# Performance work log

Measured on AMD Instinct MI355X. Metric: run time of the kernel, lower is better.

Reference implementation:

```python
import jax, jax.numpy as jnp
import numpy as np

B, D, L = 8, 512, 8192


def log_g(x):
    # th.where(x >= 0, log(relu(x) + 1), x)
    return jnp.where(x >= 0, jnp.log1p(jnp.maximum(x, 0.0)), x)


def min_gru(hg):
    # hg: [B, H, L] -> [B, H/2, L]
    h, gate = jnp.split(hg, 2, axis=1)
    log_coeffs = -jax.nn.softplus(gate)                      # log a_t
    log_values = -jax.nn.softplus(-gate) + log_g(h)          # log b_t
    a_star = jnp.cumsum(log_coeffs, axis=2)
    log_h0_plus_b_star = jax.lax.cumlogsumexp(log_values - a_star, axis=2)
    return jnp.exp(a_star + log_h0_plus_b_star)


def conv1x1(x, w, b):
    # x: [B, D, L], w: [E, D], b: [E]  (kernel-size-1 Conv1d == pointwise linear)
    return jnp.einsum('ed,bdl->bel', w, x) + b[None, :, None]


def setup_inputs() -> dict:
    key = jax.random.key(0)
    k1, k2, k3, k4, k5 = jax.random.split(key, 5)
    scale = 1.0 / np.sqrt(D)
    x = jax.random.normal(k1, (B, D, L), dtype=jnp.float32)
    w_fore = jax.random.normal(k2, (D, D), dtype=jnp.float32) * scale
    b_fore = jax.random.normal(k3, (D,), dtype=jnp.float32) * scale
    w_back = jax.random.normal(k4, (D, D), dtype=jnp.float32) * scale
    b_back = jax.random.normal(k5, (D,), dtype=jnp.float32) * scale
    return {'x': x, 'w_fore': w_fore, 'b_fore': b_fore, 'w_back': w_back, 'b_back': b_back}


def reference(x, w_fore, b_fore, w_back, b_back):
    fore = min_gru(conv1x1(x, w_fore, b_fore))                            # [B, D/2, L]
    back = jnp.flip(min_gru(conv1x1(jnp.flip(x, 2), w_back, b_back)), 2)  # [B, D/2, L]
    return jnp.concatenate([fore, back], axis=1)                          # [B, D, L]
```

## Files before the change

kernel.cpp:

```cpp
#include <hip/hip_runtime.h>

#define BATCH 8
#define DIN   512
#define SEQ   8192
#define ECH   1024
#define HCH   256
#define CL    32
#define NCHNK (SEQ / CL)
#define NSC   16

typedef __bf16 bf16;
typedef __bf16 bf16x8 __attribute__((ext_vector_type(8)));
typedef __bf16 bf16x4 __attribute__((ext_vector_type(4)));
typedef float  floatx4 __attribute__((ext_vector_type(4)));

__device__ __forceinline__ void async_ld16(void* lds, const void* g) {
  __builtin_amdgcn_global_load_lds(
      (const __attribute__((address_space(1))) unsigned int*)g,
      (__attribute__((address_space(3))) unsigned int*)lds, 16, 0, 0);
}

__device__ __forceinline__ float bits2f(unsigned u) {
  return __builtin_bit_cast(float, u);
}

__device__ __forceinline__ void gru_ab(unsigned v, float& a, float& bt) {
  float hh = bits2f(v << 16);
  float g  = bits2f(v & 0xffff0000u);
  float eg = __expf(-g);
  float sg = 1.f / (1.f + eg);
  a = eg * sg;
  float gv = hh >= 0.f ? 1.f + hh : __expf(hh);
  bt = sg * gv;
}

__global__ void k_wconv(const float* __restrict__ wf, const float* __restrict__ bfo,
                        const float* __restrict__ wb, const float* __restrict__ bb,
                        bf16* __restrict__ Wb, float* __restrict__ bias) {
  int idx = blockIdx.x * 256 + threadIdx.x;
  if (idx < ECH * DIN) {
    int n = idx >> 9, d = idx & 511;
    int dir = n >> 9, r = n & 511, e = r >> 1, isg = r & 1;
    int s = e + (isg ? HCH : 0);
    const float* w = dir ? wb : wf;
    Wb[idx] = (bf16)w[s * DIN + d];
  }
  if (idx < ECH) {
    int dir = idx >> 9, r = idx & 511, e = r >> 1, isg = r & 1;
    int s = e + (isg ? HCH : 0);
    bias[idx] = (dir ? bb : bfo)[s];
  }
}

__global__ void k_xpose(const float* __restrict__ x, bf16* __restrict__ xT) {
  __shared__ float T[64 * 65];
  int t = threadIdx.x;
  int l0 = blockIdx.x * 64;
  int d0 = blockIdx.y * 64;
  int b  = blockIdx.z;
  const float* xb = x + (size_t)b * DIN * SEQ;
#pragma unroll
  for (int p = 0; p < 4; ++p) {
    int dl = (t >> 4) + p * 16;
    int l4 = (t & 15) * 4;
    float4 v = *(const float4*)(xb + (size_t)(d0 + dl) * SEQ + l0 + l4);
    T[dl * 65 + l4 + 0] = v.x;
    T[dl * 65 + l4 + 1] = v.y;
    T[dl * 65 + l4 + 2] = v.z;
    T[dl * 65 + l4 + 3] = v.w;
  }
  __syncthreads();
  bf16* xTb = xT + (size_t)b * SEQ * DIN;
#pragma unroll
  for (int p = 0; p < 2; ++p) {
    int ll = (t >> 3) + p * 32;
    int d8 = (t & 7) * 8;
    bf16x8 h;
#pragma unroll
    for (int j = 0; j < 8; ++j) h[j] = (bf16)T[(d8 + j) * 65 + ll];
    *(bf16x8*)(xTb + (size_t)(l0 + ll) * DIN + d0 + d8) = h;
  }
}

__launch_bounds__(256, 4)
__global__ void k_gemm(const bf16* __restrict__ xT, const bf16* __restrict__ Wb,
                       const float* __restrict__ bias, bf16* __restrict__ hg,
                       float* __restrict__ Asum, float* __restrict__ Bsum) {
  __shared__ bf16 lds[16896];
  bf16* As = lds;
  bf16* Bs = lds + 8192;

  int t = threadIdx.x;
  int lane = t & 63, wave = t >> 6;

  int lin = blockIdx.x + 8 * blockIdx.y;
  int xcd = lin & 7;
  int seq = lin >> 3;
  int ltile = xcd + 8 * (seq >> 3);
  int ntile = seq & 7;
  int n0 = ntile * 128;
  int l0 = ltile * 128;
  int b  = blockIdx.z;

  int l15 = lane & 15, quad = lane >> 4;
  int wm = wave >> 1, wn = wave & 1;
  int mb = wm * 64, nb = wn * 64;

  const bf16* gA = xT + ((size_t)b * SEQ + l0) * DIN;
  const bf16* gB = Wb + (size_t)n0 * DIN;

  int srow = wave * 32 + (lane >> 3);
  int scol = (((lane & 7) ^ (lane >> 3)) * 8);

  floatx4 acc[4][4];
#pragma unroll
  for (int i = 0; i < 4; ++i)
#pragma unroll
    for (int j = 0; j < 4; ++j) acc[i][j] = (floatx4){0.f, 0.f, 0.f, 0.f};

  for (int kt = 0; kt < DIN / 64; ++kt) {
    int k0 = kt * 64;
#pragma unroll
    for (int q = 0; q < 4; ++q) {
      async_ld16(As + (wave * 32 + q * 8) * 64,
                 gA + (size_t)(srow + q * 8) * DIN + k0 + scol);
      async_ld16(Bs + (wave * 32 + q * 8) * 64,
                 gB + (size_t)(srow + q * 8) * DIN + k0 + scol);
    }
    __syncthreads();
#pragma unroll
    for (int kk = 0; kk < 64; kk += 32) {
      int rsw = l15 & 7;
      bf16x8 af[4], bfr[4];
#pragma unroll
      for (int i = 0; i < 4; ++i)
        af[i] = *(const bf16x8*)(As + (mb + i * 16 + l15) * 64 +
                                 (((kk >> 3) + quad) ^ rsw) * 8);
#pragma unroll
      for (int i = 0; i < 4; ++i)
        bfr[i] = *(const bf16x8*)(Bs + (nb + i * 16 + l15) * 64 +
                                  (((kk >> 3) + quad) ^ rsw) * 8);
#pragma unroll
      for (int mi = 0; mi < 4; ++mi)
#pragma unroll
        for (int ni = 0; ni < 4; ++ni)
          acc[mi][ni] = __builtin_amdgcn_mfma_f32_16x16x32_bf16(
              af[mi], bfr[ni], acc[mi][ni], 0, 0, 0);
    }
    __syncthreads();
  }

  float bb4[4];
#pragma unroll
  for (int ni = 0; ni < 4; ++ni) bb4[ni] = bias[n0 + nb + ni * 16 + l15];
  bf16* Cs = lds;
#pragma unroll
  for (int mi = 0; mi < 4; ++mi)
#pragma unroll
    for (int ni = 0; ni < 4; ++ni)
#pragma unroll
      for (int r = 0; r < 4; ++r) {
        int row = mb + mi * 16 + quad * 4 + r;
        int col = nb + ni * 16 + l15;
        Cs[row * 132 + col] = (bf16)(acc[mi][ni][r] + bb4[ni]);
      }
  __syncthreads();
  bf16* hgb = hg + ((size_t)b * SEQ + l0) * ECH + n0;
#pragma unroll
  for (int p = 0; p < 8; ++p) {
    int row = p * 16 + (t >> 4);
    int seg = t & 15;
    *(bf16x8*)(hgb + (size_t)row * ECH + seg * 8) =
        *(const bf16x8*)(Cs + row * 132 + seg * 8);
  }

  {
    int dirn = ntile >> 2;
    int c = wave, el = lane;
    float A = 1.f, Bc = 0.f;
#pragma unroll 8
    for (int i = 0; i < CL; ++i) {
      int row = c * CL + (dirn ? (CL - 1 - i) : i);
      unsigned v = *(const unsigned*)(Cs + row * 132 + 2 * el);
      float a, bt;
      gru_ab(v, a, bt);
      A *= a;
      Bc = a * Bc + bt;
    }
    int chunkg = ltile * 4 + c;
    int eg = ((n0 & 511) >> 1) + el;
    size_t o = ((size_t)(b * 2 + dirn) * NCHNK + chunkg) * 256 + eg;
    Asum[o] = A;
    Bsum[o] = Bc;
  }
}

__global__ void k_scan2a(const float* __restrict__ Asum, const float* __restrict__ Bsum,
                         float* __restrict__ SA, float* __restrict__ SB) {
  int e = threadIdx.x, sc = blockIdx.x, row2 = blockIdx.y, dir = row2 & 1;
  size_t base = (size_t)row2 * NCHNK;
  float Acc = 1.f, Bcc = 0.f;
#pragma unroll
  for (int i = 0; i < 16; ++i) {
    int c = sc * 16 + (dir ? 15 - i : i);
    size_t o = (base + c) * 256 + e;
    float a = Asum[o], bv = Bsum[o];
    Acc = a * Acc;
    Bcc = a * Bcc + bv;
  }
  size_t so = ((size_t)row2 * NSC + sc) * 256 + e;
  SA[so] = Acc;
  SB[so] = Bcc;
}

__global__ void k_scan2b(const float* __restrict__ SA, const float* __restrict__ SB,
                         float* __restrict__ hsc) {
  int e = threadIdx.x, row2 = blockIdx.x, dir = row2 & 1;
  float h = 0.f;
  for (int i = 0; i < NSC; ++i) {
    int sc = dir ? NSC - 1 - i : i;
    size_t o = ((size_t)row2 * NSC + sc) * 256 + e;
    hsc[o] = h;
    h = SA[o] * h + SB[o];
  }
}

__global__ void k_scan2c(const float* __restrict__ Asum, const float* __restrict__ Bsum,
                         const float* __restrict__ hsc, float* __restrict__ hin) {
  int e = threadIdx.x, sc = blockIdx.x, row2 = blockIdx.y, dir = row2 & 1;
  float h = hsc[((size_t)row2 * NSC + sc) * 256 + e];
#pragma unroll
  for (int i = 0; i < 16; ++i) {
    int c = sc * 16 + (dir ? 15 - i : i);
    size_t o = ((size_t)row2 * NCHNK + c) * 256 + e;
    hin[o] = h;
    h = Asum[o] * h + Bsum[o];
  }
}

__global__ void k_scan3(const bf16* __restrict__ hg, const float* __restrict__ hin,
                        float* __restrict__ out) {
  __shared__ float T[256 * 33];
  int t = threadIdx.x;
  int chunk = blockIdx.x, dir = blockIdx.y, b = blockIdx.z;
  const bf16* hb = hg + (size_t)b * SEQ * ECH + dir * 512 + 2 * t;
  float h = hin[((size_t)(b * 2 + dir) * NCHNK + chunk) * 256 + t];
  int lbase = chunk * CL;
#pragma unroll 8
  for (int i = 0; i < CL; ++i) {
    int ll = dir ? (CL - 1 - i) : i;
    unsigned v = *(const unsigned*)(hb + (size_t)(lbase + ll) * ECH);
    float a, bt;
    gru_ab(v, a, bt);
    h = a * h + bt;
    T[t * 33 + ll] = h;
  }
  __syncthreads();
  float* ob = out + ((size_t)b * 512 + dir * 256) * SEQ + lbase;
#pragma unroll
  for (int p = 0; p < 8; ++p) {
    int row = p * 32 + (t >> 3);
    int c4 = (t & 7) * 4;
    float4 v4;
    v4.x = T[row * 33 + c4 + 0];
    v4.y = T[row * 33 + c4 + 1];
    v4.z = T[row * 33 + c4 + 2];
    v4.w = T[row * 33 + c4 + 3];
    *(float4*)(ob + (size_t)row * SEQ + c4) = v4;
  }
}

extern "C" void kernel_launch(void* const* d_in, const int* in_sizes, int n_in,
                              void* d_out, int out_size, void* d_ws, size_t ws_size,
                              hipStream_t stream) {
  const float* x   = (const float*)d_in[0];
  const float* wf  = (const float*)d_in[1];
  const float* bfo = (const float*)d_in[2];
  const float* wb  = (const float*)d_in[3];
  const float* bb  = (const float*)d_in[4];
  float* out = (float*)d_out;
  char* ws = (char*)d_ws;

  bf16*  xT   = (bf16*)(ws);
  bf16*  hg   = (bf16*)(ws + 67108864);
  bf16*  Wbm  = (bf16*)(ws + 201326592);
  float* bias = (float*)(ws + 202375168);
  float* Asum = (float*)(ws + 202379264);
  float* Bsum = (float*)(ws + 206573568);
  float* hin  = (float*)(ws + 210767872);
  float* SA   = (float*)(ws + 214962176);
  float* SB   = (float*)(ws + 215224320);
  float* hsc  = (float*)(ws + 215486464);

  k_wconv<<<2048, 256, 0, stream>>>(wf, bfo, wb, bb, Wbm, bias);
  k_xpose<<<dim3(SEQ / 64, DIN / 64, BATCH), 256, 0, stream>>>(x, xT);
  k_gemm<<<dim3(ECH / 128, SEQ / 128, BATCH), 256, 0, stream>>>(xT, Wbm, bias, hg,
                                                                Asum, Bsum);
  k_scan2a<<<dim3(NSC, 16), 256, 0, stream>>>(Asum, Bsum, SA, SB);
  k_scan2b<<<16, 256, 0, stream>>>(SA, SB, hsc);
  k_scan2c<<<dim3(NSC, 16), 256, 0, stream>>>(Asum, Bsum, hsc, hin);
  k_scan3<<<dim3(NCHNK, 2, BATCH), 256, 0, stream>>>(hg, hin, out);
}
```

Baseline: 372.0 us.

## Enlarge GEMM tile to 256x256 with 4-stage async LDS pipeline

The GEMM kernel moves from 128x128 tiles with 256 threads and a single-buffered K loop to 256x256 tiles with 512 threads. The K loop now uses BK=32 with a 4-deep ring of LDS buffers, prefetching three stages ahead with explicit vmcnt waits and raised wave priority around the MFMAs. The aim is to overlap global loads with matrix math and to increase operand reuse per tile. In exchange it uses far more LDS and registers, which lowers occupancy. The LDS layout drops the XOR swizzle, which risks bank conflicts, and the chunk-summary epilogue is remapped to the larger tile.

```diff
diff --git a/kernel.cpp b/kernel.cpp
--- a/kernel.cpp
+++ b/kernel.cpp
@@ -11,7 +11,6 @@
 
 typedef __bf16 bf16;
 typedef __bf16 bf16x8 __attribute__((ext_vector_type(8)));
-typedef __bf16 bf16x4 __attribute__((ext_vector_type(4)));
 typedef float  floatx4 __attribute__((ext_vector_type(4)));
 
 __device__ __forceinline__ void async_ld16(void* lds, const void* g) {
@@ -82,113 +81,129 @@
   }
 }
 
-__launch_bounds__(256, 4)
+#define BKK 32
+#define NKT (DIN / BKK)
+#define CS_STRIDE 268
+
+__launch_bounds__(512, 2)
 __global__ void k_gemm(const bf16* __restrict__ xT, const bf16* __restrict__ Wb,
                        const float* __restrict__ bias, bf16* __restrict__ hg,
                        float* __restrict__ Asum, float* __restrict__ Bsum) {
-  __shared__ bf16 lds[16896];
-  bf16* As = lds;
-  bf16* Bs = lds + 8192;
+  __shared__ __align__(16) bf16 lds[68608];
 
   int t = threadIdx.x;
   int lane = t & 63, wave = t >> 6;
-
-  int lin = blockIdx.x + 8 * blockIdx.y;
-  int xcd = lin & 7;
-  int seq = lin >> 3;
-  int ltile = xcd + 8 * (seq >> 3);
-  int ntile = seq & 7;
-  int n0 = ntile * 128;
-  int l0 = ltile * 128;
+  int l15 = lane & 15, quad = lane >> 4;
+  int wm = wave >> 2, wn = wave & 3;
+
+  int lin = blockIdx.x + 4 * blockIdx.y;
+  int swz = (lin & 7) * 16 + (lin >> 3);
+  int ntile = swz & 3, ltile = swz >> 2;
+  int n0 = ntile * 256;
+  int l0 = ltile * 256;
   int b  = blockIdx.z;
-
-  int l15 = lane & 15, quad = lane >> 4;
-  int wm = wave >> 1, wn = wave & 1;
-  int mb = wm * 64, nb = wn * 64;
 
   const bf16* gA = xT + ((size_t)b * SEQ + l0) * DIN;
   const bf16* gB = Wb + (size_t)n0 * DIN;
 
-  int srow = wave * 32 + (lane >> 3);
-  int scol = (((lane & 7) ^ (lane >> 3)) * 8);
-
-  floatx4 acc[4][4];
-#pragma unroll
-  for (int i = 0; i < 4; ++i)
+  int srow = t >> 2;
+  int scol = (t & 3) * 8;
+
+  float bb4[4];
+#pragma unroll
+  for (int ni = 0; ni < 4; ++ni) bb4[ni] = bias[n0 + wn * 64 + ni * 16 + l15];
+
+#define STAGE(KT) do {                                                     \
+    bf16* dst = lds + ((KT) & 3) * 16384 + t * 8;                          \
+    const bf16* sA = gA + (size_t)srow * DIN + (KT) * BKK + scol;          \
+    const bf16* sB = gB + (size_t)srow * DIN + (KT) * BKK + scol;          \
+    async_ld16(dst,         sA);                                           \
+    async_ld16(dst + 4096,  sA + (size_t)128 * DIN);                       \
+    async_ld16(dst + 8192,  sB);                                           \
+    async_ld16(dst + 12288, sB + (size_t)128 * DIN);                       \
+  } while (0)
+
+  STAGE(0); STAGE(1); STAGE(2);
+
+  floatx4 acc[8][4];
+#pragma unroll
+  for (int i = 0; i < 8; ++i)
 #pragma unroll
     for (int j = 0; j < 4; ++j) acc[i][j] = (floatx4){0.f, 0.f, 0.f, 0.f};
 
-  for (int kt = 0; kt < DIN / 64; ++kt) {
-    int k0 = kt * 64;
-#pragma unroll
-    for (int q = 0; q < 4; ++q) {
-      async_ld16(As + (wave * 32 + q * 8) * 64,
-                 gA + (size_t)(srow + q * 8) * DIN + k0 + scol);
-      async_ld16(Bs + (wave * 32 + q * 8) * 64,
-                 gB + (size_t)(srow + q * 8) * DIN + k0 + scol);
-    }
-    __syncthreads();
-#pragma unroll
-    for (int kk = 0; kk < 64; kk += 32) {
-      int rsw = l15 & 7;
-      bf16x8 af[4], bfr[4];
-#pragma unroll
-      for (int i = 0; i < 4; ++i)
-        af[i] = *(const bf16x8*)(As + (mb + i * 16 + l15) * 64 +
-                                 (((kk >> 3) + quad) ^ rsw) * 8);
-#pragma unroll
-      for (int i = 0; i < 4; ++i)
-        bfr[i] = *(const bf16x8*)(Bs + (nb + i * 16 + l15) * 64 +
-                                  (((kk >> 3) + quad) ^ rsw) * 8);
-#pragma unroll
-      for (int mi = 0; mi < 4; ++mi)
-#pragma unroll
-        for (int ni = 0; ni < 4; ++ni)
-          acc[mi][ni] = __builtin_amdgcn_mfma_f32_16x16x32_bf16(
-              af[mi], bfr[ni], acc[mi][ni], 0, 0, 0);
-    }
-    __syncthreads();
-  }
-
-  float bb4[4];
-#pragma unroll
-  for (int ni = 0; ni < 4; ++ni) bb4[ni] = bias[n0 + nb + ni * 16 + l15];
+#pragma unroll
+  for (int kt = 0; kt < NKT; ++kt) {
+    if (kt <= NKT - 3)      asm volatile("s_waitcnt vmcnt(8)" ::: "memory");
+    else if (kt == NKT - 2) asm volatile("s_waitcnt vmcnt(4)" ::: "memory");
+    else                    asm volatile("s_waitcnt vmcnt(0)" ::: "memory");
+    __builtin_amdgcn_s_barrier();
+    asm volatile("" ::: "memory");
+
+    if (kt + 3 < NKT) STAGE(kt + 3);
+
+    const bf16* As = lds + (kt & 3) * 16384;
+    const bf16* Bs = As + 8192;
+    bf16x8 af[8], bfr[4];
+#pragma unroll
+    for (int i = 0; i < 8; ++i)
+      af[i] = *(const bf16x8*)(As + (wm * 128 + i * 16 + l15) * BKK + quad * 8);
+#pragma unroll
+    for (int i = 0; i < 4; ++i)
+      bfr[i] = *(const bf16x8*)(Bs + (wn * 64 + i * 16 + l15) * BKK + quad * 8);
+
+    __builtin_amdgcn_s_setprio(1);
+#pragma unroll
+    for (int mi = 0; mi < 8; ++mi)
+#pragma unroll
+      for (int ni = 0; ni < 4; ++ni)
+        acc[mi][ni] = __builtin_amdgcn_mfma_f32_16x16x32_bf16(
+            af[mi], bfr[ni], acc[mi][ni], 0, 0, 0);
+    __builtin_amdgcn_s_setprio(0);
+  }
+#undef STAGE
+
+  __syncthreads();
+
   bf16* Cs = lds;
 #pragma unroll
-  for (int mi = 0; mi < 4; ++mi)
+  for (int mi = 0; mi < 8; ++mi)
 #pragma unroll
     for (int ni = 0; ni < 4; ++ni)
 #pragma unroll
       for (int r = 0; r < 4; ++r) {
-        int row = mb + mi * 16 + quad * 4 + r;
-        int col = nb + ni * 16 + l15;
-        Cs[row * 132 + col] = (bf16)(acc[mi][ni][r] + bb4[ni]);
+        int row = wm * 128 + mi * 16 + quad * 4 + r;
+        int col = wn * 64 + ni * 16 + l15;
+        Cs[row * CS_STRIDE + col] = (bf16)(acc[mi][ni][r] + bb4[ni]);
       }
   __syncthreads();
+
   bf16* hgb = hg + ((size_t)b * SEQ + l0) * ECH + n0;
 #pragma unroll
-  for (int p = 0; p < 8; ++p) {
-    int row = p * 16 + (t >> 4);
-    int seg = t & 15;
+  for (int p = 0; p < 16; ++p) {
+    int row = p * 16 + (t >> 5);
+    int seg = t & 31;
     *(bf16x8*)(hgb + (size_t)row * ECH + seg * 8) =
-        *(const bf16x8*)(Cs + row * 132 + seg * 8);
-  }
-
-  {
-    int dirn = ntile >> 2;
-    int c = wave, el = lane;
+        *(const bf16x8*)(Cs + row * CS_STRIDE + seg * 8);
+  }
+
+  int dirn = ntile >> 1;
+#pragma unroll
+  for (int j = 0; j < 2; ++j) {
+    int u = t + j * 512;
+    int c = u >> 7;
+    int e = u & 127;
     float A = 1.f, Bc = 0.f;
 #pragma unroll 8
     for (int i = 0; i < CL; ++i) {
       int row = c * CL + (dirn ? (CL - 1 - i) : i);
-      unsigned v = *(const unsigned*)(Cs + row * 132 + 2 * el);
+      unsigned v = *(const unsigned*)(Cs + row * CS_STRIDE + 2 * e);
       float a, bt;
       gru_ab(v, a, bt);
       A *= a;
       Bc = a * Bc + bt;
     }
-    int chunkg = ltile * 4 + c;
-    int eg = ((n0 & 511) >> 1) + el;
+    int chunkg = ltile * 8 + c;
+    int eg = (ntile & 1) * 128 + e;
     size_t o = ((size_t)(b * 2 + dirn) * NCHNK + chunkg) * 256 + eg;
     Asum[o] = A;
     Bsum[o] = Bc;
@@ -294,7 +309,7 @@
 
   k_wconv<<<2048, 256, 0, stream>>>(wf, bfo, wb, bb, Wbm, bias);
   k_xpose<<<dim3(SEQ / 64, DIN / 64, BATCH), 256, 0, stream>>>(x, xT);
-  k_gemm<<<dim3(ECH / 128, SEQ / 128, BATCH), 256, 0, stream>>>(xT, Wbm, bias, hg,
+  k_gemm<<<dim3(ECH / 256, SEQ / 256, BATCH), 512, 0, stream>>>(xT, Wbm, bias, hg,
                                                                 Asum, Bsum);
   k_scan2a<<<dim3(NSC, 16), 256, 0, stream>>>(Asum, Bsum, SA, SB);
   k_scan2b<<<16, 256, 0, stream>>>(SA, SB, hsc);
```

Result: slower. 390.2 us (+4.9%).

## Load pre-fragmented weights directly to registers and merge scan kernels into one

Applied to the files above, without the earlier changes.

The weight conversion kernel now writes W in an MFMA-fragment-ordered layout, so the GEMM loads B operands from global straight into registers instead of staging them through LDS. The LDS traffic and async loads for W are removed. The K loop is fully unrolled and the bias load is hoisted ahead of it. The three-kernel hierarchical chunk scan is replaced by one sequential kernel over all 256 chunks, with only 16 blocks. That saves two launches but makes a long serial loop with little parallelism.

```diff
diff --git a/kernel.cpp b/kernel.cpp
--- a/kernel.cpp
+++ b/kernel.cpp
@@ -11,7 +11,6 @@
 
 typedef __bf16 bf16;
 typedef __bf16 bf16x8 __attribute__((ext_vector_type(8)));
-typedef __bf16 bf16x4 __attribute__((ext_vector_type(4)));
 typedef float  floatx4 __attribute__((ext_vector_type(4)));
 
 __device__ __forceinline__ void async_ld16(void* lds, const void* g) {
@@ -36,14 +35,16 @@
 
 __global__ void k_wconv(const float* __restrict__ wf, const float* __restrict__ bfo,
                         const float* __restrict__ wb, const float* __restrict__ bb,
-                        bf16* __restrict__ Wb, float* __restrict__ bias) {
+                        bf16* __restrict__ Wf, float* __restrict__ bias) {
   int idx = blockIdx.x * 256 + threadIdx.x;
   if (idx < ECH * DIN) {
     int n = idx >> 9, d = idx & 511;
     int dir = n >> 9, r = n & 511, e = r >> 1, isg = r & 1;
     int s = e + (isg ? HCH : 0);
     const float* w = dir ? wb : wf;
-    Wb[idx] = (bf16)w[s * DIN + d];
+    size_t o = ((size_t)((n >> 4) * 16 + (d >> 5)) << 9) +
+               ((((d >> 3) & 3) * 16 + (n & 15)) << 3) + (d & 7);
+    Wf[o] = (bf16)w[s * DIN + d];
   }
   if (idx < ECH) {
     int dir = idx >> 9, r = idx & 511, e = r >> 1, isg = r & 1;
@@ -82,16 +83,21 @@
   }
 }
 
+#define BKK 64
+#define NKT (DIN / BKK)
+
 __launch_bounds__(256, 4)
-__global__ void k_gemm(const bf16* __restrict__ xT, const bf16* __restrict__ Wb,
+__global__ void k_gemm(const bf16* __restrict__ xT, const bf16* __restrict__ Wf,
                        const float* __restrict__ bias, bf16* __restrict__ hg,
                        float* __restrict__ Asum, float* __restrict__ Bsum) {
-  __shared__ bf16 lds[16896];
+  __shared__ __align__(16) bf16 lds[16896];
   bf16* As = lds;
-  bf16* Bs = lds + 8192;
 
   int t = threadIdx.x;
   int lane = t & 63, wave = t >> 6;
+  int l15 = lane & 15, quad = lane >> 4, rsw = l15 & 7;
+  int wm = wave >> 1, wn = wave & 1;
+  int mb = wm * 64, nb = wn * 64;
 
   int lin = blockIdx.x + 8 * blockIdx.y;
   int xcd = lin & 7;
@@ -102,15 +108,15 @@
   int l0 = ltile * 128;
   int b  = blockIdx.z;
 
-  int l15 = lane & 15, quad = lane >> 4;
-  int wm = wave >> 1, wn = wave & 1;
-  int mb = wm * 64, nb = wn * 64;
-
   const bf16* gA = xT + ((size_t)b * SEQ + l0) * DIN;
-  const bf16* gB = Wb + (size_t)n0 * DIN;
+  int nb16 = (n0 >> 4) + wn * 4;
+
+  float bb4[4];
+#pragma unroll
+  for (int ni = 0; ni < 4; ++ni) bb4[ni] = bias[n0 + nb + ni * 16 + l15];
 
   int srow = wave * 32 + (lane >> 3);
-  int scol = (((lane & 7) ^ (lane >> 3)) * 8);
+  int scol = ((lane & 7) ^ ((lane >> 3) & 7)) * 8;
 
   floatx4 acc[4][4];
 #pragma unroll
@@ -118,41 +124,41 @@
 #pragma unroll
     for (int j = 0; j < 4; ++j) acc[i][j] = (floatx4){0.f, 0.f, 0.f, 0.f};
 
-  for (int kt = 0; kt < DIN / 64; ++kt) {
-    int k0 = kt * 64;
-#pragma unroll
-    for (int q = 0; q < 4; ++q) {
+#pragma unroll
+  for (int kt = 0; kt < NKT; ++kt) {
+    int k0 = kt * BKK;
+#pragma unroll
+    for (int q = 0; q < 4; ++q)
       async_ld16(As + (wave * 32 + q * 8) * 64,
                  gA + (size_t)(srow + q * 8) * DIN + k0 + scol);
-      async_ld16(Bs + (wave * 32 + q * 8) * 64,
-                 gB + (size_t)(srow + q * 8) * DIN + k0 + scol);
+
+    bf16x8 bfr[4][2];
+#pragma unroll
+    for (int i = 0; i < 4; ++i)
+#pragma unroll
+      for (int k2 = 0; k2 < 2; ++k2)
+        bfr[i][k2] = *(const bf16x8*)(Wf +
+            (((size_t)(nb16 + i) * 16 + kt * 2 + k2) << 9) + lane * 8);
+
+    __syncthreads();
+
+#pragma unroll
+    for (int k2 = 0; k2 < 2; ++k2) {
+      bf16x8 af[4];
+#pragma unroll
+      for (int i = 0; i < 4; ++i)
+        af[i] = *(const bf16x8*)(As + (mb + i * 16 + l15) * 64 +
+                                 (((k2 * 4 + quad) ^ rsw) * 8));
+#pragma unroll
+      for (int mi = 0; mi < 4; ++mi)
+#pragma unroll
+        for (int ni = 0; ni < 4; ++ni)
+          acc[mi][ni] = __builtin_amdgcn_mfma_f32_16x16x32_bf16(
+              af[mi], bfr[ni][k2], acc[mi][ni], 0, 0, 0);
     }
     __syncthreads();
-#pragma unroll
-    for (int kk = 0; kk < 64; kk += 32) {
-      int rsw = l15 & 7;
-      bf16x8 af[4], bfr[4];
-#pragma unroll
-      for (int i = 0; i < 4; ++i)
-        af[i] = *(const bf16x8*)(As + (mb + i * 16 + l15) * 64 +
-                                 (((kk >> 3) + quad) ^ rsw) * 8);
-#pragma unroll
-      for (int i = 0; i < 4; ++i)
-        bfr[i] = *(const bf16x8*)(Bs + (nb + i * 16 + l15) * 64 +
-                                  (((kk >> 3) + quad) ^ rsw) * 8);
-#pragma unroll
-      for (int mi = 0; mi < 4; ++mi)
-#pragma unroll
-        for (int ni = 0; ni < 4; ++ni)
-          acc[mi][ni] = __builtin_amdgcn_mfma_f32_16x16x32_bf16(
-              af[mi], bfr[ni], acc[mi][ni], 0, 0, 0);
-    }
-    __syncthreads();
-  }
-
-  float bb4[4];
-#pragma unroll
-  for (int ni = 0; ni < 4; ++ni) bb4[ni] = bias[n0 + nb + ni * 16 + l15];
+  }
+
   bf16* Cs = lds;
 #pragma unroll
   for (int mi = 0; mi < 4; ++mi)
@@ -195,44 +201,15 @@
   }
 }
 
-__global__ void k_scan2a(const float* __restrict__ Asum, const float* __restrict__ Bsum,
-                         float* __restrict__ SA, float* __restrict__ SB) {
-  int e = threadIdx.x, sc = blockIdx.x, row2 = blockIdx.y, dir = row2 & 1;
+__global__ void k_scan2(const float* __restrict__ Asum, const float* __restrict__ Bsum,
+                        float* __restrict__ hin) {
+  int e = threadIdx.x, row2 = blockIdx.x, dir = row2 & 1;
   size_t base = (size_t)row2 * NCHNK;
-  float Acc = 1.f, Bcc = 0.f;
-#pragma unroll
-  for (int i = 0; i < 16; ++i) {
-    int c = sc * 16 + (dir ? 15 - i : i);
+  float h = 0.f;
+#pragma unroll 8
+  for (int i = 0; i < NCHNK; ++i) {
+    int c = dir ? (NCHNK - 1 - i) : i;
     size_t o = (base + c) * 256 + e;
-    float a = Asum[o], bv = Bsum[o];
-    Acc = a * Acc;
-    Bcc = a * Bcc + bv;
-  }
-  size_t so = ((size_t)row2 * NSC + sc) * 256 + e;
-  SA[so] = Acc;
-  SB[so] = Bcc;
-}
-
-__global__ void k_scan2b(const float* __restrict__ SA, const float* __restrict__ SB,
-                         float* __restrict__ hsc) {
-  int e = threadIdx.x, row2 = blockIdx.x, dir = row2 & 1;
-  float h = 0.f;
-  for (int i = 0; i < NSC; ++i) {
-    int sc = dir ? NSC - 1 - i : i;
-    size_t o = ((size_t)row2 * NSC + sc) * 256 + e;
-    hsc[o] = h;
-    h = SA[o] * h + SB[o];
-  }
-}
-
-__global__ void k_scan2c(const float* __restrict__ Asum, const float* __restrict__ Bsum,
-                         const float* __restrict__ hsc, float* __restrict__ hin) {
-  int e = threadIdx.x, sc = blockIdx.x, row2 = blockIdx.y, dir = row2 & 1;
-  float h = hsc[((size_t)row2 * NSC + sc) * 256 + e];
-#pragma unroll
-  for (int i = 0; i < 16; ++i) {
-    int c = sc * 16 + (dir ? 15 - i : i);
-    size_t o = ((size_t)row2 * NCHNK + c) * 256 + e;
     hin[o] = h;
     h = Asum[o] * h + Bsum[o];
   }
@@ -283,21 +260,16 @@
 
   bf16*  xT   = (bf16*)(ws);
   bf16*  hg   = (bf16*)(ws + 67108864);
-  bf16*  Wbm  = (bf16*)(ws + 201326592);
+  bf16*  Wfm  = (bf16*)(ws + 201326592);
   float* bias = (float*)(ws + 202375168);
   float* Asum = (float*)(ws + 202379264);
   float* Bsum = (float*)(ws + 206573568);
   float* hin  = (float*)(ws + 210767872);
-  float* SA   = (float*)(ws + 214962176);
-  float* SB   = (float*)(ws + 215224320);
-  float* hsc  = (float*)(ws + 215486464);
-
-  k_wconv<<<2048, 256, 0, stream>>>(wf, bfo, wb, bb, Wbm, bias);
+
+  k_wconv<<<2048, 256, 0, stream>>>(wf, bfo, wb, bb, Wfm, bias);
   k_xpose<<<dim3(SEQ / 64, DIN / 64, BATCH), 256, 0, stream>>>(x, xT);
-  k_gemm<<<dim3(ECH / 128, SEQ / 128, BATCH), 256, 0, stream>>>(xT, Wbm, bias, hg,
+  k_gemm<<<dim3(ECH / 128, SEQ / 128, BATCH), 256, 0, stream>>>(xT, Wfm, bias, hg,
                                                                 Asum, Bsum);
-  k_scan2a<<<dim3(NSC, 16), 256, 0, stream>>>(Asum, Bsum, SA, SB);
-  k_scan2b<<<16, 256, 0, stream>>>(SA, SB, hsc);
-  k_scan2c<<<dim3(NSC, 16), 256, 0, stream>>>(Asum, Bsum, hsc, hin);
+  k_scan2<<<16, 256, 0, stream>>>(Asum, Bsum, hin);
   k_scan3<<<dim3(NCHNK, 2, BATCH), 256, 0, stream>>>(hg, hin, out);
 }
```

New measurement: 497.4 us. 33.7% more time.

## Pre-swizzle weights into MFMA fragment layout and read B operand directly from global

Applied to the files above, without the earlier changes.

The weight conversion now writes W in a per-16-row fragment order, so each GEMM wave can load its B operands straight from global/L2 into registers instead of staging them through LDS. The K tile grows to 128, with only the activation tile staged in a 16-way XOR-swizzled LDS layout, and B loads for the second half are issued between MFMA batches. The weight conversion and the x transpose are merged into one launch to save a kernel launch. The cost is more register pressure (launch bounds drop to 3 waves per SIMD) and global-latency exposure on the B loads.

```diff
diff --git a/kernel.cpp b/kernel.cpp
--- a/kernel.cpp
+++ b/kernel.cpp
@@ -11,7 +11,6 @@
 
 typedef __bf16 bf16;
 typedef __bf16 bf16x8 __attribute__((ext_vector_type(8)));
-typedef __bf16 bf16x4 __attribute__((ext_vector_type(4)));
 typedef float  floatx4 __attribute__((ext_vector_type(4)));
 
 __device__ __forceinline__ void async_ld16(void* lds, const void* g) {
@@ -34,30 +33,36 @@
   bt = sg * gv;
 }
 
-__global__ void k_wconv(const float* __restrict__ wf, const float* __restrict__ bfo,
-                        const float* __restrict__ wb, const float* __restrict__ bb,
-                        bf16* __restrict__ Wb, float* __restrict__ bias) {
-  int idx = blockIdx.x * 256 + threadIdx.x;
-  if (idx < ECH * DIN) {
-    int n = idx >> 9, d = idx & 511;
-    int dir = n >> 9, r = n & 511, e = r >> 1, isg = r & 1;
-    int s = e + (isg ? HCH : 0);
-    const float* w = dir ? wb : wf;
-    Wb[idx] = (bf16)w[s * DIN + d];
-  }
-  if (idx < ECH) {
-    int dir = idx >> 9, r = idx & 511, e = r >> 1, isg = r & 1;
-    int s = e + (isg ? HCH : 0);
-    bias[idx] = (dir ? bb : bfo)[s];
-  }
-}
-
-__global__ void k_xpose(const float* __restrict__ x, bf16* __restrict__ xT) {
+__global__ void k_prep(const float* __restrict__ x,
+                       const float* __restrict__ wf, const float* __restrict__ bfo,
+                       const float* __restrict__ wb, const float* __restrict__ bb,
+                       bf16* __restrict__ xT, bf16* __restrict__ Wf,
+                       float* __restrict__ bias) {
   __shared__ float T[64 * 65];
+  int bid = blockIdx.x;
   int t = threadIdx.x;
-  int l0 = blockIdx.x * 64;
-  int d0 = blockIdx.y * 64;
-  int b  = blockIdx.z;
+  if (bid < 2048) {
+    int idx = bid * 256 + t;
+    if (idx < ECH * DIN) {
+      int n = idx >> 9, d = idx & 511;
+      int dir = n >> 9, r = n & 511, e = r >> 1, isg = r & 1;
+      int s = e + (isg ? HCH : 0);
+      const float* w = dir ? wb : wf;
+      size_t o = ((size_t)((n >> 4) * 16 + (d >> 5)) << 9) +
+                 ((((d >> 3) & 3) * 16 + (n & 15)) << 3) + (d & 7);
+      Wf[o] = (bf16)w[s * DIN + d];
+    }
+    if (idx < ECH) {
+      int dir = idx >> 9, r = idx & 511, e = r >> 1, isg = r & 1;
+      int s = e + (isg ? HCH : 0);
+      bias[idx] = (dir ? bb : bfo)[s];
+    }
+    return;
+  }
+  int id = bid - 2048;
+  int l0 = (id & 127) * 64;
+  int d0 = ((id >> 7) & 7) * 64;
+  int b  = id >> 10;
   const float* xb = x + (size_t)b * DIN * SEQ;
 #pragma unroll
   for (int p = 0; p < 4; ++p) {
@@ -82,16 +87,21 @@
   }
 }
 
-__launch_bounds__(256, 4)
-__global__ void k_gemm(const bf16* __restrict__ xT, const bf16* __restrict__ Wb,
+#define BKK 128
+#define NKT (DIN / BKK)
+
+__launch_bounds__(256, 3)
+__global__ void k_gemm(const bf16* __restrict__ xT, const bf16* __restrict__ Wf,
                        const float* __restrict__ bias, bf16* __restrict__ hg,
                        float* __restrict__ Asum, float* __restrict__ Bsum) {
-  __shared__ bf16 lds[16896];
+  __shared__ __align__(16) bf16 lds[16896];
   bf16* As = lds;
-  bf16* Bs = lds + 8192;
 
   int t = threadIdx.x;
   int lane = t & 63, wave = t >> 6;
+  int l15 = lane & 15, quad = lane >> 4;
+  int wm = wave >> 1, wn = wave & 1;
+  int mb = wm * 64, nb = wn * 64;
 
   int lin = blockIdx.x + 8 * blockIdx.y;
   int xcd = lin & 7;
@@ -102,15 +112,12 @@
   int l0 = ltile * 128;
   int b  = blockIdx.z;
 
-  int l15 = lane & 15, quad = lane >> 4;
-  int wm = wave >> 1, wn = wave & 1;
-  int mb = wm * 64, nb = wn * 64;
-
   const bf16* gA = xT + ((size_t)b * SEQ + l0) * DIN;
-  const bf16* gB = Wb + (size_t)n0 * DIN;
-
-  int srow = wave * 32 + (lane >> 3);
-  int scol = (((lane & 7) ^ (lane >> 3)) * 8);
+  int nb16 = (n0 >> 4) + wn * 4;
+
+  float bb4[4];
+#pragma unroll
+  for (int ni = 0; ni < 4; ++ni) bb4[ni] = bias[n0 + nb + ni * 16 + l15];
 
   floatx4 acc[4][4];
 #pragma unroll
@@ -118,41 +125,65 @@
 #pragma unroll
     for (int j = 0; j < 4; ++j) acc[i][j] = (floatx4){0.f, 0.f, 0.f, 0.f};
 
-  for (int kt = 0; kt < DIN / 64; ++kt) {
-    int k0 = kt * 64;
-#pragma unroll
-    for (int q = 0; q < 4; ++q) {
-      async_ld16(As + (wave * 32 + q * 8) * 64,
-                 gA + (size_t)(srow + q * 8) * DIN + k0 + scol);
-      async_ld16(Bs + (wave * 32 + q * 8) * 64,
-                 gB + (size_t)(srow + q * 8) * DIN + k0 + scol);
-    }
+#pragma unroll
+  for (int kt = 0; kt < NKT; ++kt) {
+    int k0 = kt * BKK;
+#pragma unroll
+    for (int j = 0; j < 8; ++j) {
+      int i_ = t + j * 256;
+      int row_ = i_ >> 4, slot_ = i_ & 15;
+      async_ld16(As + (size_t)i_ * 8,
+                 gA + (size_t)row_ * DIN + k0 + ((slot_ ^ (row_ & 15)) * 8));
+    }
+
+    bf16x8 bfr[4][2];
+#pragma unroll
+    for (int i = 0; i < 4; ++i)
+#pragma unroll
+      for (int k2 = 0; k2 < 2; ++k2)
+        bfr[i][k2] = *(const bf16x8*)(Wf +
+            (((size_t)(nb16 + i) * 16 + kt * 4 + k2) << 9) + lane * 8);
+
     __syncthreads();
-#pragma unroll
-    for (int kk = 0; kk < 64; kk += 32) {
-      int rsw = l15 & 7;
-      bf16x8 af[4], bfr[4];
+
+#pragma unroll
+    for (int k2 = 0; k2 < 2; ++k2) {
+      bf16x8 af[4];
 #pragma unroll
       for (int i = 0; i < 4; ++i)
-        af[i] = *(const bf16x8*)(As + (mb + i * 16 + l15) * 64 +
-                                 (((kk >> 3) + quad) ^ rsw) * 8);
-#pragma unroll
-      for (int i = 0; i < 4; ++i)
-        bfr[i] = *(const bf16x8*)(Bs + (nb + i * 16 + l15) * 64 +
-                                  (((kk >> 3) + quad) ^ rsw) * 8);
+        af[i] = *(const bf16x8*)(As + (size_t)(mb + i * 16 + l15) * 128 +
+                                 (((k2 * 4 + quad) ^ l15) * 8));
 #pragma unroll
       for (int mi = 0; mi < 4; ++mi)
 #pragma unroll
         for (int ni = 0; ni < 4; ++ni)
           acc[mi][ni] = __builtin_amdgcn_mfma_f32_16x16x32_bf16(
-              af[mi], bfr[ni], acc[mi][ni], 0, 0, 0);
+              af[mi], bfr[ni][k2], acc[mi][ni], 0, 0, 0);
+    }
+
+#pragma unroll
+    for (int i = 0; i < 4; ++i)
+#pragma unroll
+      for (int k2 = 0; k2 < 2; ++k2)
+        bfr[i][k2] = *(const bf16x8*)(Wf +
+            (((size_t)(nb16 + i) * 16 + kt * 4 + 2 + k2) << 9) + lane * 8);
+#pragma unroll
+    for (int k2 = 0; k2 < 2; ++k2) {
+      bf16x8 af[4];
+#pragma unroll
+      for (int i = 0; i < 4; ++i)
+        af[i] = *(const bf16x8*)(As + (size_t)(mb + i * 16 + l15) * 128 +
+                                 ((((k2 + 2) * 4 + quad) ^ l15) * 8));
+#pragma unroll
+      for (int mi = 0; mi < 4; ++mi)
+#pragma unroll
+        for (int ni = 0; ni < 4; ++ni)
+          acc[mi][ni] = __builtin_amdgcn_mfma_f32_16x16x32_bf16(
+              af[mi], bfr[ni][k2], acc[mi][ni], 0, 0, 0);
     }
     __syncthreads();
   }
 
-  float bb4[4];
-#pragma unroll
-  for (int ni = 0; ni < 4; ++ni) bb4[ni] = bias[n0 + nb + ni * 16 + l15];
   bf16* Cs = lds;
 #pragma unroll
   for (int mi = 0; mi < 4; ++mi)
@@ -283,7 +314,7 @@
 
   bf16*  xT   = (bf16*)(ws);
   bf16*  hg   = (bf16*)(ws + 67108864);
-  bf16*  Wbm  = (bf16*)(ws + 201326592);
+  bf16*  Wfm  = (bf16*)(ws + 201326592);
   float* bias = (float*)(ws + 202375168);
   float* Asum = (float*)(ws + 202379264);
   float* Bsum = (float*)(ws + 206573568);
@@ -292,9 +323,8 @@
   float* SB   = (float*)(ws + 215224320);
   float* hsc  = (float*)(ws + 215486464);
 
-  k_wconv<<<2048, 256, 0, stream>>>(wf, bfo, wb, bb, Wbm, bias);
-  k_xpose<<<dim3(SEQ / 64, DIN / 64, BATCH), 256, 0, stream>>>(x, xT);
-  k_gemm<<<dim3(ECH / 128, SEQ / 128, BATCH), 256, 0, stream>>>(xT, Wbm, bias, hg,
+  k_prep<<<10240, 256, 0, stream>>>(x, wf, bfo, wb, bb, xT, Wfm, bias);
+  k_gemm<<<dim3(ECH / 128, SEQ / 128, BATCH), 256, 0, stream>>>(xT, Wfm, bias, hg,
                                                                 Asum, Bsum);
   k_scan2a<<<dim3(NSC, 16), 256, 0, stream>>>(Asum, Bsum, SA, SB);
   k_scan2b<<<16, 256, 0, stream>>>(SA, SB, hsc);
```

Result: slower. 387.2 us (+4.1%).
